# Kernel tuning notes

Hardware: AMD Instinct MI355X
Metric: run time of the kernel (lower is better)

## Reference

```python
import jax, jax.numpy as jnp
import numpy as np

N_NODES = 50000
N_EDGES = 800000
N_GRAPHS = 512
D = 128


def _gcn_layer(x, W, b, src, dst, norm):
    # PyG GCNConv: h = x @ W; out[i] = sum_{j->i} norm_ji * h[j]; out += b
    h = x @ W                                   # [N, D]
    msg = h[src] * norm[:, None]                # [E+N, D] gathered messages
    out = jax.ops.segment_sum(msg, dst, num_segments=N_NODES)
    return out + b


def setup_inputs() -> dict:
    key = jax.random.key(0)
    ks = jax.random.split(key, 9)
    inp = {
        "x": jax.random.normal(ks[0], (N_NODES, D), dtype=jnp.float32),
        "W1": jax.random.normal(ks[1], (D, D), dtype=jnp.float32) * 0.05,
        "b1": jax.random.normal(ks[2], (D,), dtype=jnp.float32) * 0.05,
        "W2": jax.random.normal(ks[3], (D, D), dtype=jnp.float32) * 0.05,
        "b2": jax.random.normal(ks[4], (D,), dtype=jnp.float32) * 0.05,
        "W3": jax.random.normal(ks[5], (D, D), dtype=jnp.float32) * 0.05,
        "b3": jax.random.normal(ks[6], (D,), dtype=jnp.float32) * 0.05,
        "edge_index": jax.random.randint(ks[7], (2, N_EDGES), 0, N_NODES, dtype=jnp.int64),
        "batch_vec": jnp.sort(jax.random.randint(ks[8], (N_NODES,), 0, N_GRAPHS, dtype=jnp.int64)),
    }
    return inp


def reference(x, W1, b1, W2, b2, W3, b3, edge_index, batch_vec):
    # Add self-loops (GCNConv default) and compute symmetric normalization.
    loops = jnp.arange(N_NODES, dtype=edge_index.dtype)
    src = jnp.concatenate([edge_index[0], loops])   # [E+N]
    dst = jnp.concatenate([edge_index[1], loops])   # [E+N]
    deg = jax.ops.segment_sum(jnp.ones_like(dst, dtype=x.dtype), dst,
                              num_segments=N_NODES)
    dis = jnp.where(deg > 0, jax.lax.rsqrt(jnp.maximum(deg, 1.0)), 0.0)
    norm = dis[src] * dis[dst]                      # [E+N]

    h = jax.nn.relu(_gcn_layer(x, W1, b1, src, dst, norm))
    h = jax.nn.relu(_gcn_layer(h, W2, b2, src, dst, norm))
    h = jax.nn.relu(_gcn_layer(h, W3, b3, src, dst, norm))

    # global_add_pool: per-graph sum over nodes.
    return jax.ops.segment_sum(h, batch_vec, num_segments=N_GRAPHS)  # [G, D]
```

## Files before the change

kernel.cpp:

```cpp
#include <hip/hip_runtime.h>

#define N_NODES 50000
#define N_EDGES 800000
#define N_GRAPHS 512
#define DIM 128
#define N_PAD 50048

#define BW_LOG 9
#define BWID 512
#define NB ((N_NODES + BWID - 1) / BWID)
#define CHUNK 4096
#define NCHUNK ((N_EDGES + CHUNK - 1) / CHUNK)

typedef unsigned int uint;
typedef unsigned short ushort;
typedef __attribute__((ext_vector_type(8))) short bf16x8;
typedef __attribute__((ext_vector_type(4))) float f32x4;

__device__ __forceinline__ ushort f2bf(float f) {
    uint u = __float_as_uint(f);
    return (ushort)((u + 0x7fffu + ((u >> 16) & 1u)) >> 16);
}
__device__ __forceinline__ float bf2f(ushort h) { return __uint_as_float((uint)h << 16); }
__device__ __forceinline__ float bflo(uint p) { return __uint_as_float(p << 16); }
__device__ __forceinline__ float bfhi(uint p) { return __uint_as_float(p & 0xffff0000u); }


__global__ __launch_bounds__(256) void bhist_k(const int* __restrict__ dst,
                                               int* __restrict__ bcnt_pad, int e) {
    __shared__ int h[NB];
    int t = threadIdx.x;
    for (int i = t; i < NB; i += 256) h[i] = 0;
    __syncthreads();
    int base = blockIdx.x * CHUNK;
    for (int i = t; i < CHUNK; i += 256) {
        int idx = base + i;
        if (idx < e) atomicAdd(&h[dst[idx] >> BW_LOG], 1);
    }
    __syncthreads();
    for (int i = t; i < NB; i += 256)
        if (h[i]) atomicAdd(&bcnt_pad[i << 4], h[i]);
}

__global__ void bscan_k(const int* __restrict__ bcnt_pad, int* __restrict__ bbase,
                        int* __restrict__ bcur_pad) {
    __shared__ int v[128];
    int t = threadIdx.x;
    int x = (t < NB) ? bcnt_pad[t << 4] : 0;
    v[t] = x;
    __syncthreads();
    for (int o = 1; o < 128; o <<= 1) {
        int val = v[t];
        int add = (t >= o) ? v[t - o] : 0;
        __syncthreads();
        v[t] = val + add;
        __syncthreads();
    }
    if (t < NB) {
        int excl = (t == 0) ? 0 : v[t - 1];
        bbase[t] = excl;
        bcur_pad[t << 4] = excl;
    }
    if (t == NB - 1) bbase[NB] = v[t];
}

__global__ __launch_bounds__(256) void bscat_k(const int* __restrict__ src,
                                               const int* __restrict__ dst,
                                               int* __restrict__ bcur_pad,
                                               uint* __restrict__ stage, int e) {
    __shared__ int h[NB];
    __shared__ int bb[NB];
    __shared__ int lc[NB];
    int t = threadIdx.x;
    for (int i = t; i < NB; i += 256) h[i] = 0;
    __syncthreads();
    int base = blockIdx.x * CHUNK;
    for (int i = t; i < CHUNK; i += 256) {
        int idx = base + i;
        if (idx < e) atomicAdd(&h[dst[idx] >> BW_LOG], 1);
    }
    __syncthreads();
    for (int i = t; i < NB; i += 256) {
        int c = h[i];
        bb[i] = c ? atomicAdd(&bcur_pad[i << 4], c) : 0;
        lc[i] = 0;
    }
    __syncthreads();
    for (int i = t; i < CHUNK; i += 256) {
        int idx = base + i;
        if (idx < e) {
            int d = dst[idx];
            int b = d >> BW_LOG;
            int r = atomicAdd(&lc[b], 1);
            stage[bb[b] + r] = ((uint)src[idx] << BW_LOG) | (uint)(d & (BWID - 1));
        }
    }
}

__global__ __launch_bounds__(256) void csr_k(const uint* __restrict__ stage,
                                             const int* __restrict__ bbase,
                                             int* __restrict__ row_ptr,
                                             float* __restrict__ dis,
                                             int* __restrict__ col) {
    __shared__ int hist[BWID];
    __shared__ int excl[BWID];
    __shared__ int ws[256];
    int b = blockIdx.x, t = threadIdx.x;
    int beg = bbase[b], end = bbase[b + 1];
    for (int i = t; i < BWID; i += 256) hist[i] = 0;
    __syncthreads();
    for (int i = beg + t; i < end; i += 256)
        atomicAdd(&hist[stage[i] & (BWID - 1)], 1);
    __syncthreads();
    int s = hist[2 * t] + hist[2 * t + 1];
    ws[t] = s;
    __syncthreads();
    for (int o = 1; o < 256; o <<= 1) {
        int v = ws[t];
        int add = (t >= o) ? ws[t - o] : 0;
        __syncthreads();
        ws[t] = v + add;
        __syncthreads();
    }
    int pre = (t == 0) ? 0 : ws[t - 1];
    excl[2 * t] = pre;
    excl[2 * t + 1] = pre + hist[2 * t];
    __syncthreads();
    int node0 = b * BWID;
    for (int i = t; i < BWID; i += 256) {
        int node = node0 + i;
        if (node < N_NODES) {
            row_ptr[node] = beg + excl[i];
            dis[node] = rsqrtf((float)(hist[i] + 1));
        } else if (node == N_NODES) {
            row_ptr[node] = beg + excl[i];
        }
    }
    __syncthreads();
    for (int i = t; i < BWID; i += 256) hist[i] = excl[i];
    __syncthreads();
    for (int i = beg + t; i < end; i += 256) {
        uint p = stage[i];
        int d9 = p & (BWID - 1);
        int r = atomicAdd(&hist[d9], 1);
        col[beg + r] = (int)(p >> BW_LOG);
    }
}


__global__ void wconv_k(const float* __restrict__ Wa, const float* __restrict__ Wb,
                        const float* __restrict__ Wc, ushort* __restrict__ Whi,
                        ushort* __restrict__ Wlo) {
    int i = blockIdx.x * 256 + threadIdx.x;
    int layer = i >> 14, r = i & 16383;
    const float* W = layer == 0 ? Wa : (layer == 1 ? Wb : Wc);
    int k = r >> 7, nn = r & 127;
    float w = W[r];
    ushort h = f2bf(w);
    size_t o = (size_t)layer * DIM * DIM + nn * 128 + k;
    Whi[o] = h;
    Wlo[o] = f2bf(w - bf2f(h));
}


template <typename TIn>
__global__ __launch_bounds__(256) void gemm_mfma_k(const TIn* __restrict__ X,
                                                   const ushort* __restrict__ Whi,
                                                   const ushort* __restrict__ Wlo,
                                                   ushort* __restrict__ H, int n) {
    __shared__ __align__(16) ushort lds[128 * 136];
    int t = threadIdx.x;

    auto stageW = [&](const ushort* Wsw) {
#pragma unroll
        for (int j = 0; j < 8; j++) {
            int idx8 = t + j * 256;
            int nn = idx8 >> 4;
            int k0 = (idx8 & 15) * 8;
            uint4 v = ((const uint4*)Wsw)[idx8];
            *(uint4*)&lds[nn * 136 + k0] = v;
        }
    };

    stageW(Whi);

    int w = t >> 6, l = t & 63;
    int quad = l >> 4, lr = l & 15;
    int arow = blockIdx.x * 64 + w * 16 + lr;
    int srow = arow < n ? arow : n - 1;

    bf16x8 a[4], alo[4];
#pragma unroll
    for (int q = 0; q < 4; q++) {
        if constexpr (sizeof(TIn) == 4) {
            const float4* xp = (const float4*)(X + (size_t)srow * DIM + q * 32 + quad * 8);
            float4 v0 = xp[0], v1 = xp[1];
            float f[8] = {v0.x, v0.y, v0.z, v0.w, v1.x, v1.y, v1.z, v1.w};
            bf16x8 ah, al;
#pragma unroll
            for (int j = 0; j < 8; j++) {
                ushort h = f2bf(f[j]);
                ah[j] = (short)h;
                al[j] = (short)f2bf(f[j] - bf2f(h));
            }
            a[q] = ah;
            alo[q] = al;
        } else {
            a[q] = *(const bf16x8*)(X + (size_t)srow * DIM + q * 32 + quad * 8);
        }
    }

    f32x4 acc[8];
#pragma unroll
    for (int c = 0; c < 8; c++) acc[c] = (f32x4){0.f, 0.f, 0.f, 0.f};

    __syncthreads();
#pragma unroll
    for (int q = 0; q < 4; q++) {
#pragma unroll
        for (int c = 0; c < 8; c++) {
            bf16x8 b = *(const bf16x8*)&lds[(c * 16 + lr) * 136 + q * 32 + quad * 8];
            acc[c] = __builtin_amdgcn_mfma_f32_16x16x32_bf16(a[q], b, acc[c], 0, 0, 0);
            if constexpr (sizeof(TIn) == 4)
                acc[c] = __builtin_amdgcn_mfma_f32_16x16x32_bf16(alo[q], b, acc[c], 0, 0, 0);
        }
    }

    __syncthreads();
    stageW(Wlo);
    __syncthreads();
#pragma unroll
    for (int q = 0; q < 4; q++) {
#pragma unroll
        for (int c = 0; c < 8; c++) {
            bf16x8 b = *(const bf16x8*)&lds[(c * 16 + lr) * 136 + q * 32 + quad * 8];
            acc[c] = __builtin_amdgcn_mfma_f32_16x16x32_bf16(a[q], b, acc[c], 0, 0, 0);
        }
    }

    __syncthreads();
#pragma unroll
    for (int c = 0; c < 8; c++) {
#pragma unroll
        for (int r = 0; r < 4; r++) {
            int rl = w * 16 + quad * 4 + r;
            lds[rl * 136 + c * 16 + lr] = f2bf(acc[c][r]);
        }
    }
    __syncthreads();
#pragma unroll
    for (int j = 0; j < 4; j++) {
        int idx = t + j * 256;
        int rl = idx >> 4, sl = idx & 15;
        int grow = blockIdx.x * 64 + rl;
        if (grow < n) {
            uint4 v = *(const uint4*)&lds[rl * 136 + sl * 8];
            ((uint4*)(H + (size_t)grow * DIM))[sl] = v;
        }
    }
}


#define AGG_EDGE8(E0, PRED)                                                      \
    {                                                                            \
        int c_[8];                                                               \
        float w_[8];                                                             \
        uint4 p_[8];                                                             \
        _Pragma("unroll") for (int j = 0; j < 8; j++) {                          \
            int idx = E0 + j;                                                    \
            if (PRED) idx = idx < end ? idx : end - 1;                           \
            c_[j] = col[idx];                                                    \
        }                                                                        \
        _Pragma("unroll") for (int j = 0; j < 8; j++) {                          \
            float wv = dis[c_[j]];                                               \
            if (PRED) wv = (E0 + j < end) ? wv : 0.f;                            \
            w_[j] = wv;                                                          \
            p_[j] = *(const uint4*)(Hl + (size_t)c_[j] * DIM);                   \
        }                                                                        \
        _Pragma("unroll") for (int j = 0; j < 8; j++) {                          \
            a0 += w_[j] * bflo(p_[j].x);                                         \
            a1 += w_[j] * bfhi(p_[j].x);                                         \
            a2 += w_[j] * bflo(p_[j].y);                                         \
            a3 += w_[j] * bfhi(p_[j].y);                                         \
            a4 += w_[j] * bflo(p_[j].z);                                         \
            a5 += w_[j] * bfhi(p_[j].z);                                         \
            a6 += w_[j] * bflo(p_[j].w);                                         \
            a7 += w_[j] * bfhi(p_[j].w);                                         \
        }                                                                        \
    }

#define AGG_BODY                                                                 \
    const ushort* Hl = H + lane * 8;                                             \
    float dn = dis[node];                                                        \
    int beg = row_ptr[node], end = row_ptr[node + 1];                            \
    uint4 pw = *(const uint4*)(Hl + (size_t)node * DIM);                         \
    a0 = dn * bflo(pw.x); a1 = dn * bfhi(pw.x);                                  \
    a2 = dn * bflo(pw.y); a3 = dn * bfhi(pw.y);                                  \
    a4 = dn * bflo(pw.z); a5 = dn * bfhi(pw.z);                                  \
    a6 = dn * bflo(pw.w); a7 = dn * bfhi(pw.w);                                  \
    int e = beg;                                                                 \
    for (; e + 7 < end; e += 8) AGG_EDGE8(e, 0)                                  \
    if (e < end) AGG_EDGE8(e, 1)                                                 \
    a0 = fmaxf(a0 * dn + bias[d0], 0.f);                                         \
    a1 = fmaxf(a1 * dn + bias[d0 + 1], 0.f);                                     \
    a2 = fmaxf(a2 * dn + bias[d0 + 2], 0.f);                                     \
    a3 = fmaxf(a3 * dn + bias[d0 + 3], 0.f);                                     \
    a4 = fmaxf(a4 * dn + bias[d0 + 4], 0.f);                                     \
    a5 = fmaxf(a5 * dn + bias[d0 + 5], 0.f);                                     \
    a6 = fmaxf(a6 * dn + bias[d0 + 6], 0.f);                                     \
    a7 = fmaxf(a7 * dn + bias[d0 + 7], 0.f);

__global__ __launch_bounds__(256) void agg_k(const ushort* __restrict__ H,
                                             const int* __restrict__ row_ptr,
                                             const int* __restrict__ col,
                                             const float* __restrict__ dis,
                                             const float* __restrict__ bias,
                                             ushort* __restrict__ Out, int n) {
    int node = blockIdx.x * 16 + (threadIdx.x >> 4);
    int lane = threadIdx.x & 15;
    if (node >= n) return;
    int d0 = lane * 8;
    float a0, a1, a2, a3, a4, a5, a6, a7;
    AGG_BODY
    uint4 o;
    o.x = (uint)f2bf(a0) | ((uint)f2bf(a1) << 16);
    o.y = (uint)f2bf(a2) | ((uint)f2bf(a3) << 16);
    o.z = (uint)f2bf(a4) | ((uint)f2bf(a5) << 16);
    o.w = (uint)f2bf(a6) | ((uint)f2bf(a7) << 16);
    *(uint4*)(Out + (size_t)node * DIM + d0) = o;
}

__global__ __launch_bounds__(256) void agg_pool_k(const ushort* __restrict__ H,
                                                  const int* __restrict__ row_ptr,
                                                  const int* __restrict__ col,
                                                  const float* __restrict__ dis,
                                                  const float* __restrict__ bias,
                                                  const int* __restrict__ batch,
                                                  float* __restrict__ Out, int n) {
    __shared__ float acc[DIM];
    int t = threadIdx.x;
    int node = blockIdx.x * 16 + (t >> 4);
    int lane = t & 15;
    int d0 = lane * 8;
    float a0 = 0.f, a1 = 0.f, a2 = 0.f, a3 = 0.f, a4 = 0.f, a5 = 0.f, a6 = 0.f, a7 = 0.f;
    int g = -1;
    if (node < n) {
        AGG_BODY
        g = batch[node];
    }
    int first = blockIdx.x * 16;
    int last = first + 15 < n ? first + 15 : n - 1;
    int g0 = batch[first], g1 = batch[last];
    for (int gr = g0; gr <= g1; gr++) {
        if (t < DIM) acc[t] = 0.f;
        __syncthreads();
        if (g == gr) {
            atomicAdd(&acc[d0], a0);
            atomicAdd(&acc[d0 + 1], a1);
            atomicAdd(&acc[d0 + 2], a2);
            atomicAdd(&acc[d0 + 3], a3);
            atomicAdd(&acc[d0 + 4], a4);
            atomicAdd(&acc[d0 + 5], a5);
            atomicAdd(&acc[d0 + 6], a6);
            atomicAdd(&acc[d0 + 7], a7);
        }
        __syncthreads();
        if (t < DIM) atomicAdd(&Out[gr * DIM + t], acc[t]);
        __syncthreads();
    }
}


extern "C" void kernel_launch(void* const* d_in, const int* in_sizes, int n_in,
                              void* d_out, int out_size, void* d_ws, size_t ws_size,
                              hipStream_t stream) {
    const float* x  = (const float*)d_in[0];
    const float* W1 = (const float*)d_in[1];
    const float* b1 = (const float*)d_in[2];
    const float* W2 = (const float*)d_in[3];
    const float* b2 = (const float*)d_in[4];
    const float* W3 = (const float*)d_in[5];
    const float* b3 = (const float*)d_in[6];
    const int*   ei = (const int*)d_in[7];
    const int*   bv = (const int*)d_in[8];
    float* out = (float*)d_out;

    const int N = N_NODES, E = N_EDGES;

    char* p = (char*)d_ws;
    auto alloc = [&](size_t bytes) -> void* {
        void* r = (void*)p;
        p += (bytes + 255) & ~(size_t)255;
        return r;
    };
    int*    bcnt_pad = (int*)alloc((size_t)NB * 16 * 4);
    int*    bcur_pad = (int*)alloc((size_t)NB * 16 * 4);
    int*    bbase    = (int*)alloc((size_t)(NB + 1) * 4);
    int*    row_ptr  = (int*)alloc((size_t)(N + 1) * 4);
    float*  dis      = (float*)alloc((size_t)N * 4);
    uint*   stage    = (uint*)alloc((size_t)E * 4);
    int*    col      = (int*)alloc((size_t)E * 4);
    ushort* B1       = (ushort*)alloc((size_t)N_PAD * DIM * 2);
    ushort* B2       = (ushort*)alloc((size_t)N_PAD * DIM * 2);

    ushort* Whi = (ushort*)stage;
    ushort* Wlo = Whi + (size_t)3 * DIM * DIM;

    const int* src = ei;
    const int* dst = ei + E;

    hipMemsetAsync(d_out, 0, (size_t)N_GRAPHS * DIM * sizeof(float), stream);
    hipMemsetAsync(bcnt_pad, 0, (size_t)NB * 16 * 4, stream);

    bhist_k<<<NCHUNK, 256, 0, stream>>>(dst, bcnt_pad, E);
    bscan_k<<<1, 128, 0, stream>>>(bcnt_pad, bbase, bcur_pad);
    bscat_k<<<NCHUNK, 256, 0, stream>>>(src, dst, bcur_pad, stage, E);
    csr_k<<<NB, 256, 0, stream>>>(stage, bbase, row_ptr, dis, col);

    wconv_k<<<192, 256, 0, stream>>>(W1, W2, W3, Whi, Wlo);

    int gemm_grid = N_PAD / 64;
    int agg_grid  = (N + 15) / 16;

    gemm_mfma_k<float><<<gemm_grid, 256, 0, stream>>>(x, Whi, Wlo, B1, N);
    agg_k<<<agg_grid, 256, 0, stream>>>(B1, row_ptr, col, dis, b1, B2, N);

    gemm_mfma_k<ushort><<<gemm_grid, 256, 0, stream>>>(B2, Whi + (size_t)DIM * DIM,
                                                       Wlo + (size_t)DIM * DIM, B1, N);
    agg_k<<<agg_grid, 256, 0, stream>>>(B1, row_ptr, col, dis, b2, B2, N);

    gemm_mfma_k<ushort><<<gemm_grid, 256, 0, stream>>>(B2, Whi + (size_t)2 * DIM * DIM,
                                                       Wlo + (size_t)2 * DIM * DIM, B1, N);
    agg_pool_k<<<agg_grid, 256, 0, stream>>>(B1, row_ptr, col, dis, b3, bv, out, N);
}
```

Measured before the change: 283.4 us.

## Pre-scale GEMM output by source degree norm and stage CSR columns in LDS

Result: slower. 289.5 us (+2.1%).

```diff
diff --git a/kernel.cpp b/kernel.cpp
--- a/kernel.cpp
+++ b/kernel.cpp
@@ -167,6 +167,7 @@
 __global__ __launch_bounds__(256) void gemm_mfma_k(const TIn* __restrict__ X,
                                                    const ushort* __restrict__ Whi,
                                                    const ushort* __restrict__ Wlo,
+                                                   const float* __restrict__ dis,
                                                    ushort* __restrict__ H, int n) {
     __shared__ __align__(16) ushort lds[128 * 136];
     int t = threadIdx.x;
@@ -238,13 +239,22 @@
         }
     }
 
+    float dsc[4];
+    int orow0 = blockIdx.x * 64 + w * 16 + quad * 4;
+#pragma unroll
+    for (int r = 0; r < 4; r++) {
+        int rr = orow0 + r;
+        if (rr > n - 1) rr = n - 1;
+        dsc[r] = dis[rr];
+    }
+
     __syncthreads();
 #pragma unroll
     for (int c = 0; c < 8; c++) {
 #pragma unroll
         for (int r = 0; r < 4; r++) {
             int rl = w * 16 + quad * 4 + r;
-            lds[rl * 136 + c * 16 + lr] = f2bf(acc[c][r]);
+            lds[rl * 136 + c * 16 + lr] = f2bf(acc[c][r] * dsc[r]);
         }
     }
     __syncthreads();
@@ -261,6 +271,18 @@
 }
 
 
+#define COLCAP 1024
+
+#define AGG_STAGE                                                                \
+    int first_n = blockIdx.x * 16;                                               \
+    int cbase = row_ptr[first_n];                                                \
+    int last_n = first_n + 16;                                                   \
+    if (last_n > n) last_n = n;                                                  \
+    int ccnt = row_ptr[last_n] - cbase;                                          \
+    if (ccnt > COLCAP) ccnt = COLCAP;                                            \
+    for (int i = threadIdx.x; i < ccnt; i += 256) cols_s[i] = col[cbase + i];    \
+    __syncthreads();
+
 #define AGG_EDGE8(E0, PRED)                                                      \
     {                                                                            \
         int c_[8];                                                               \
@@ -268,13 +290,15 @@
         uint4 p_[8];                                                             \
         _Pragma("unroll") for (int j = 0; j < 8; j++) {                          \
             int idx = E0 + j;                                                    \
-            if (PRED) idx = idx < end ? idx : end - 1;                           \
-            c_[j] = col[idx];                                                    \
+            w_[j] = 1.f;                                                         \
+            if (PRED) {                                                          \
+                w_[j] = (idx < end) ? 1.f : 0.f;                                 \
+                idx = idx < end ? idx : end - 1;                                 \
+            }                                                                    \
+            int li = idx - cbase;                                                \
+            c_[j] = (li < COLCAP) ? cols_s[li] : col[idx];                       \
         }                                                                        \
         _Pragma("unroll") for (int j = 0; j < 8; j++) {                          \
-            float wv = dis[c_[j]];                                               \
-            if (PRED) wv = (E0 + j < end) ? wv : 0.f;                            \
-            w_[j] = wv;                                                          \
             p_[j] = *(const uint4*)(Hl + (size_t)c_[j] * DIM);                   \
         }                                                                        \
         _Pragma("unroll") for (int j = 0; j < 8; j++) {                          \
@@ -294,10 +318,10 @@
     float dn = dis[node];                                                        \
     int beg = row_ptr[node], end = row_ptr[node + 1];                            \
     uint4 pw = *(const uint4*)(Hl + (size_t)node * DIM);                         \
-    a0 = dn * bflo(pw.x); a1 = dn * bfhi(pw.x);                                  \
-    a2 = dn * bflo(pw.y); a3 = dn * bfhi(pw.y);                                  \
-    a4 = dn * bflo(pw.z); a5 = dn * bfhi(pw.z);                                  \
-    a6 = dn * bflo(pw.w); a7 = dn * bfhi(pw.w);                                  \
+    a0 = bflo(pw.x); a1 = bfhi(pw.x);                                            \
+    a2 = bflo(pw.y); a3 = bfhi(pw.y);                                            \
+    a4 = bflo(pw.z); a5 = bfhi(pw.z);                                            \
+    a6 = bflo(pw.w); a7 = bfhi(pw.w);                                            \
     int e = beg;                                                                 \
     for (; e + 7 < end; e += 8) AGG_EDGE8(e, 0)                                  \
     if (e < end) AGG_EDGE8(e, 1)                                                 \
@@ -316,8 +340,10 @@
                                              const float* __restrict__ dis,
                                              const float* __restrict__ bias,
                                              ushort* __restrict__ Out, int n) {
+    __shared__ int cols_s[COLCAP];
     int node = blockIdx.x * 16 + (threadIdx.x >> 4);
     int lane = threadIdx.x & 15;
+    AGG_STAGE
     if (node >= n) return;
     int d0 = lane * 8;
     float a0, a1, a2, a3, a4, a5, a6, a7;
@@ -338,11 +364,13 @@
                                                   const int* __restrict__ batch,
                                                   float* __restrict__ Out, int n) {
     __shared__ float acc[DIM];
+    __shared__ int cols_s[COLCAP];
     int t = threadIdx.x;
     int node = blockIdx.x * 16 + (t >> 4);
     int lane = t & 15;
     int d0 = lane * 8;
     float a0 = 0.f, a1 = 0.f, a2 = 0.f, a3 = 0.f, a4 = 0.f, a5 = 0.f, a6 = 0.f, a7 = 0.f;
+    AGG_STAGE
     int g = -1;
     if (node < n) {
         AGG_BODY
@@ -422,14 +450,14 @@
     int gemm_grid = N_PAD / 64;
     int agg_grid  = (N + 15) / 16;
 
-    gemm_mfma_k<float><<<gemm_grid, 256, 0, stream>>>(x, Whi, Wlo, B1, N);
+    gemm_mfma_k<float><<<gemm_grid, 256, 0, stream>>>(x, Whi, Wlo, dis, B1, N);
     agg_k<<<agg_grid, 256, 0, stream>>>(B1, row_ptr, col, dis, b1, B2, N);
 
     gemm_mfma_k<ushort><<<gemm_grid, 256, 0, stream>>>(B2, Whi + (size_t)DIM * DIM,
-                                                       Wlo + (size_t)DIM * DIM, B1, N);
+                                                       Wlo + (size_t)DIM * DIM, dis, B1, N);
     agg_k<<<agg_grid, 256, 0, stream>>>(B1, row_ptr, col, dis, b2, B2, N);
 
     gemm_mfma_k<ushort><<<gemm_grid, 256, 0, stream>>>(B2, Whi + (size_t)2 * DIM * DIM,
-                                                       Wlo + (size_t)2 * DIM * DIM, B1, N);
+                                                       Wlo + (size_t)2 * DIM * DIM, dis, B1, N);
     agg_pool_k<<<agg_grid, 256, 0, stream>>>(B1, row_ptr, col, dis, b3, bv, out, N);
 }
```
